# Optimization experiments

Measured on AMD Instinct MI355X. Metric: run time of the kernel, lower is better.

Reference implementation:

```python
import jax, jax.numpy as jnp
import numpy as np

K_MIN = 30.0
TAU = 1e-06
BETA = 0.9
LAMBDA_MAX = 0.1
LAMBDA_SCALE = 1.0

N, D_OUT, N_MODULES, N_CONTEXTS = 262144, 128, 64, 16


def setup_inputs() -> dict:
    key = jax.random.key(0)
    k1, k2, k3, k4 = jax.random.split(key, 4)
    Y_hat = jax.random.normal(k1, (N, D_OUT), dtype=jnp.float32)
    context_weights = jax.random.uniform(k2, (N, N_CONTEXTS), dtype=jnp.float32)
    M_pinv = jax.random.normal(k3, (N_MODULES, D_OUT), dtype=jnp.float32) * 0.1
    C_prior = jax.random.normal(k4, (N_CONTEXTS, N_MODULES, N_MODULES), dtype=jnp.float32) * 0.1
    # Buffers exactly as registered in __init__
    ema_Sigma = jnp.broadcast_to(jnp.eye(N_MODULES, dtype=jnp.float32), (N_CONTEXTS, N_MODULES, N_MODULES))
    ema_sigma_sq = jnp.ones((N_CONTEXTS, N_MODULES), dtype=jnp.float32)
    ema_initialized = jnp.zeros((N_CONTEXTS,), dtype=bool)
    return {"Y_hat": Y_hat, "context_weights": context_weights, "M_pinv": M_pinv,
            "C_prior": C_prior, "ema_Sigma": ema_Sigma, "ema_sigma_sq": ema_sigma_sq,
            "ema_initialized": ema_initialized}


def reference(Y_hat, context_weights, M_pinv, C_prior, ema_Sigma, ema_sigma_sq, ema_initialized):
    # Z_hat: [N, m]
    Z = Y_hat @ M_pinv.T
    wsum = context_weights.sum(axis=0)            # [T] == eff_n per context
    active = wsum >= K_MIN                        # context skipping, vectorized
    # Weighted mean per context: [T, m]
    mu = (context_weights.T @ Z) / wsum[:, None]
    # Weighted covariance: sum_n w_norm * (z-mu)(z-mu)^T == E_w[zz^T] - mu mu^T
    w_norm = context_weights / wsum[None, :]      # [N, T]
    S = jnp.einsum('nt,nm,nk->tmk', w_norm, Z, Z)  # [T, m, m]
    Sigma = S - mu[:, :, None] * mu[:, None, :]
    # EMA sigma_sq update (no-grad in original -> stop_gradient)
    Sigma_sg = jax.lax.stop_gradient(Sigma)
    diag_init = jnp.diagonal(Sigma_sg, axis1=1, axis2=2)                       # first-call branch
    diag_ema = jnp.diagonal(BETA * ema_Sigma + (1.0 - BETA) * Sigma_sg, axis1=1, axis2=2)
    sigma_sq = jnp.where(ema_initialized[:, None], diag_ema, diag_init)        # [T, m]
    std = jnp.sqrt(sigma_sq + TAU)
    denom = std[:, :, None] * std[:, None, :]
    C_hat = jnp.clip(Sigma / (denom + TAU), -1.0, 1.0)
    loss_t = jnp.sum((C_hat - C_prior) ** 2, axis=(1, 2)) / wsum               # [T]
    n_active = jnp.sum(active)
    total = jnp.sum(jnp.where(active, loss_t, 0.0))
    total = jnp.where(n_active > 0,
                      LAMBDA_MAX * LAMBDA_SCALE * total / jnp.maximum(n_active, 1).astype(total.dtype),
                      jnp.zeros((), total.dtype))
    return total
```

## Files before the change

### kernel.cpp

```cpp
#include <hip/hip_runtime.h>
#include <stdint.h>

#define N_ROWS 262144
#define D_OUTC 128
#define M_MOD  64
#define T_CTX  16

#define ZB_OFF   ((size_t)0)
#define ZB_BYTES ((size_t)M_MOD * N_ROWS * 2)
#define WT_OFF   (ZB_OFF + ZB_BYTES)
#define WT_BYTES ((size_t)T_CTX * N_ROWS * 2)
#define SS_OFF   (WT_OFF + WT_BYTES)
#define SS_BYTES ((size_t)T_CTX * M_MOD * M_MOD * 4)
#define B_OFF    (SS_OFF + SS_BYTES)
#define B_BYTES  ((size_t)T_CTX * M_MOD * 4)
#define WSUM_OFF (B_OFF + B_BYTES)
#define WSUM_BYTES ((size_t)64)
#define LT_OFF   (WSUM_OFF + WSUM_BYTES)
#define LT_BYTES ((size_t)64)
#define PSS_OFF  (LT_OFF + LT_BYTES)
#define PSS_BYTES ((size_t)256 * T_CTX * M_MOD * M_MOD * 2)
#define NEED_BIG (PSS_OFF + PSS_BYTES)

typedef __attribute__((ext_vector_type(4))) float f32x4;
typedef __attribute__((ext_vector_type(8))) _Float16 f16x8;
typedef __attribute__((ext_vector_type(2))) _Float16 h2;

union FR { uint4 u; f16x8 v; h2 h[4]; };

__device__ __forceinline__ float bf2f(unsigned short u) {
  return __uint_as_float(((unsigned int)u) << 16);
}
__device__ __forceinline__ unsigned short f2bf(float f) {
  unsigned int x = __float_as_uint(f);
  return (unsigned short)((x + 0x7fffu + ((x >> 16) & 1u)) >> 16);
}
__device__ __forceinline__ h2 cvt_pkrtz(float a, float b) {
  return __builtin_bit_cast(h2, __builtin_amdgcn_cvt_pkrtz(a, b));
}
#if __has_builtin(__builtin_amdgcn_fdot2)
__device__ __forceinline__ float fdot2f(h2 a, h2 b, float c) {
  return __builtin_amdgcn_fdot2(a, b, c, false);
}
#else
__device__ __forceinline__ float fdot2f(h2 a, h2 b, float c) {
  return c + (float)a[0] * (float)b[0] + (float)a[1] * (float)b[1];
}
#endif

#define WAITVM(N) asm volatile("s_waitcnt vmcnt(" #N ")" ::: "memory")
#define SBAR() do { __builtin_amdgcn_s_barrier(); __builtin_amdgcn_sched_barrier(0); } while (0)

__global__ __launch_bounds__(256, 3) void zk_kernel(
    const float* __restrict__ Y, const float* __restrict__ Mp,
    const float* __restrict__ W,
    _Float16* __restrict__ Zbt, _Float16* __restrict__ Wt)
{
  __shared__ __align__(16) float    Yl[64 * 128];
  __shared__ __align__(16) _Float16 Mpl[64 * 128];
  __shared__ float Wf[16][65];
  const int tid  = threadIdx.x;
  const int l    = tid & 63;
  const int wv   = tid >> 6;
  const int g    = l >> 4;
  const int col  = l & 15;
  const int n0   = blockIdx.x * 64;

#pragma unroll
  for (int k = 0; k < 8; ++k) {
    const int pr  = wv * 8 + k;
    const int row = pr * 2 + (l >> 5);
    const int q   = l & 31;
    const int b   = (q & ~7) | ((q & 7) ^ (row & 7));
    const float* src = Y + ((size_t)(n0 + row)) * D_OUTC + b * 4;
    __builtin_amdgcn_global_load_lds((const unsigned int*)src,
        (unsigned int*)((char*)&Yl[0] + pr * 1024), 16, 0, 0);
  }
  {
    const int m  = tid >> 2;
    const int dq = tid & 3;
#pragma unroll
    for (int i = 0; i < 4; ++i) {
      const int s = dq * 4 + i;
      const float* mp = Mp + (size_t)m * D_OUTC + s * 8;
      float4 a = *(const float4*)mp;
      float4 b = *(const float4*)(mp + 4);
      FR o;
      o.h[0] = cvt_pkrtz(a.x, a.y); o.h[1] = cvt_pkrtz(a.z, a.w);
      o.h[2] = cvt_pkrtz(b.x, b.y); o.h[3] = cvt_pkrtz(b.z, b.w);
      const int ss = (s & ~7) | ((s & 7) ^ (m & 7));
      *(uint4*)((char*)&Mpl[0] + m * 256 + ss * 16) = o.u;
    }
  }
  {
    const int r  = tid >> 2;
    const int c0 = (tid & 3) * 4;
    float4 wv4 = *(const float4*)(W + (size_t)(n0 + r) * T_CTX + c0);
    Wf[c0 + 0][r] = wv4.x; Wf[c0 + 1][r] = wv4.y;
    Wf[c0 + 2][r] = wv4.z; Wf[c0 + 3][r] = wv4.w;
  }
  __syncthreads();
  {
    const int t = tid >> 4, ni = tid & 15;
    h2 h0 = cvt_pkrtz(Wf[t][4 * ni], Wf[t][4 * ni + 1]);
    h2 h1 = cvt_pkrtz(Wf[t][4 * ni + 2], Wf[t][4 * ni + 3]);
    uint2 pk = {__builtin_bit_cast(unsigned int, h0), __builtin_bit_cast(unsigned int, h1)};
    *(uint2*)(Wt + (size_t)t * N_ROWS + n0 + 4 * ni) = pk;
  }
  f32x4 acc[4];
#pragma unroll
  for (int qi = 0; qi < 4; ++qi) acc[qi] = (f32x4){0.f, 0.f, 0.f, 0.f};
  const int nrow = wv * 16 + col;
#pragma unroll
  for (int ks = 0; ks < 4; ++ks) {
    const char* yb = (const char*)&Yl[0] + nrow * 512 + ks * 128;
    uint4 y0 = *(const uint4*)(yb + 16 * ((2 * g) ^ (nrow & 7)));
    uint4 y1 = *(const uint4*)(yb + 16 * ((2 * g + 1) ^ (nrow & 7)));
    const float* f0 = (const float*)&y0;
    const float* f1 = (const float*)&y1;
    FR B;
    B.h[0] = cvt_pkrtz(f0[0], f0[1]); B.h[1] = cvt_pkrtz(f0[2], f0[3]);
    B.h[2] = cvt_pkrtz(f1[0], f1[1]); B.h[3] = cvt_pkrtz(f1[2], f1[3]);
#pragma unroll
    for (int qi = 0; qi < 4; ++qi) {
      const int m = qi * 16 + col;
      const int s = ks * 4 + g;
      FR A;
      A.u = *(const uint4*)((char*)&Mpl[0] + m * 256 + 16 * ((s & ~7) | ((s & 7) ^ (m & 7))));
      acc[qi] = __builtin_amdgcn_mfma_f32_16x16x32_f16(A.v, B.v, acc[qi], 0, 0, 0);
    }
  }
#pragma unroll
  for (int qi = 0; qi < 4; ++qi)
#pragma unroll
    for (int i = 0; i < 4; ++i)
      Zbt[(size_t)(qi * 16 + g * 4 + i) * N_ROWS + n0 + wv * 16 + col] =
          (_Float16)acc[qi][i];
}

#define SS_NS 256
#define NCH   16
template <bool PARTIAL>
__global__ __launch_bounds__(512, 4) void ss_kernel(
    const _Float16* __restrict__ Zbt, const _Float16* __restrict__ Wt,
    float* __restrict__ SS, float* __restrict__ Bm,
    unsigned short* __restrict__ Pss)
{
  __shared__ __align__(16) _Float16 Zl[4][64 * 64];
  __shared__ __align__(16) _Float16 Wlds[8 * 1024];
  const int tid = threadIdx.x;
  const int l   = tid & 63;
  const int wv  = tid >> 6;
  const int g   = l >> 4;
  const int col = l & 15;
  const int ns  = blockIdx.x & (SS_NS - 1);
  const int cg  = blockIdx.x >> 8;
  const int ctx = cg * 8 + wv;
  const int n0b = ns * 1024;

  f32x4 acc[4][4];
  f32x4 accB[4];
#pragma unroll
  for (int a = 0; a < 4; ++a) {
    accB[a] = (f32x4){0.f, 0.f, 0.f, 0.f};
#pragma unroll
    for (int b = 0; b < 4; ++b) acc[a][b] = (f32x4){0.f, 0.f, 0.f, 0.f};
  }
  FR ones;
#pragma unroll
  for (int j = 0; j < 4; ++j) ones.h[j] = (h2){(_Float16)1.f, (_Float16)1.f};

#pragma unroll
  for (int k = 0; k < 2; ++k) {
    const _Float16* wsrc = Wt + (size_t)ctx * N_ROWS + n0b + k * 512 + l * 8;
    __builtin_amdgcn_global_load_lds((const unsigned int*)wsrc,
        (unsigned int*)((char*)&Wlds[0] + wv * 2048 + k * 1024), 16, 0, 0);
  }
  const int zrow  = 8 * wv + (l >> 3);
  const int zslot = l & 7;
  auto stage = [&](int c) {
    const int n0 = n0b + c * 64;
    const _Float16* src = Zbt + (size_t)zrow * N_ROWS + n0 + 8 * (zslot ^ (zrow & 7));
    __builtin_amdgcn_global_load_lds((const unsigned int*)src,
        (unsigned int*)((char*)&Zl[c & 3][0] + wv * 1024 + l * 16), 16, 0, 0);
  };

  stage(0); stage(1); stage(2);
  WAITVM(2);
  SBAR();

  for (int c = 0; c < NCH; ++c) {
    if (c + 3 < NCH) stage(c + 3);
    const char* zb = (const char*)&Zl[c & 3][0];
    const char* wb = (const char*)&Wlds[0] + wv * 2048 + c * 128;
#pragma unroll
    for (int s = 0; s < 2; ++s) {
      FR wfr;
      wfr.u = *(const uint4*)(wb + s * 64 + g * 16);
      FR fr[4];
#pragma unroll
      for (int qi = 0; qi < 4; ++qi) {
        const int r = qi * 16 + col;
        fr[qi].u = *(const uint4*)(zb + r * 128 + 16 * ((s * 4 + g) ^ (r & 7)));
      }
      __builtin_amdgcn_s_setprio(1);
#pragma unroll
      for (int qi = 0; qi < 4; ++qi) {
        FR A;
#pragma unroll
        for (int j = 0; j < 4; ++j) A.h[j] = fr[qi].h[j] * wfr.h[j];
        accB[qi] = __builtin_amdgcn_mfma_f32_16x16x32_f16(A.v, ones.v, accB[qi], 0, 0, 0);
#pragma unroll
        for (int ki = 0; ki < 4; ++ki)
          acc[qi][ki] = __builtin_amdgcn_mfma_f32_16x16x32_f16(A.v, fr[ki].v, acc[qi][ki], 0, 0, 0);
      }
      __builtin_amdgcn_s_setprio(0);
    }
    if (c + 3 < NCH)      { WAITVM(2); SBAR(); }
    else if (c == NCH - 3) { WAITVM(1); SBAR(); }
    else if (c == NCH - 2) { WAITVM(0); SBAR(); }
  }

  if (col == 0) {
#pragma unroll
    for (int qi = 0; qi < 4; ++qi)
#pragma unroll
      for (int i = 0; i < 4; ++i)
        atomicAdd(&Bm[ctx * 64 + qi * 16 + g * 4 + i], accB[qi][i]);
  }
  if (PARTIAL) {
    unsigned short* P = Pss + ((size_t)ns * 16 + ctx) * 4096;
#pragma unroll
    for (int qi = 0; qi < 4; ++qi)
#pragma unroll
      for (int ki = 0; ki < 4; ++ki)
#pragma unroll
        for (int i = 0; i < 4; ++i)
          P[(qi * 16 + g * 4 + i) * 64 + ki * 16 + col] = f2bf(acc[qi][ki][i]);
  } else {
#pragma unroll
    for (int qi = 0; qi < 4; ++qi)
#pragma unroll
      for (int ki = 0; ki < 4; ++ki)
#pragma unroll
        for (int i = 0; i < 4; ++i)
          atomicAdd(&SS[(size_t)ctx * 4096 + (qi * 16 + g * 4 + i) * 64 + ki * 16 + col],
                    acc[qi][ki][i]);
  }
}

__global__ __launch_bounds__(256) void wsk_kernel(const _Float16* __restrict__ Wt,
                                                  float* __restrict__ wsum)
{
  const int tid = threadIdx.x;
  const int t = blockIdx.x >> 2, q = blockIdx.x & 3;
  const uint4* base = (const uint4*)(Wt + (size_t)t * N_ROWS + q * 65536);
  const h2 one2 = {(_Float16)1.f, (_Float16)1.f};
  float s = 0.f;
  for (int i = tid; i < 8192; i += 256) {
    uint4 v = base[i];
    const h2* h = (const h2*)&v;
#pragma unroll
    for (int j = 0; j < 4; ++j) s = fdot2f(h[j], one2, s);
  }
  s += __shfl_xor(s, 1);  s += __shfl_xor(s, 2);
  s += __shfl_xor(s, 4);  s += __shfl_xor(s, 8);
  s += __shfl_xor(s, 16); s += __shfl_xor(s, 32);
  __shared__ float red[4];
  if ((tid & 63) == 0) red[tid >> 6] = s;
  __syncthreads();
  if (tid == 0) atomicAdd(&wsum[t], red[0] + red[1] + red[2] + red[3]);
}

__global__ __launch_bounds__(256) void ssred_kernel(
    const unsigned short* __restrict__ Pss, float* __restrict__ SS)
{
  const int e = blockIdx.x * 256 + threadIdx.x;
  float s = 0.f;
#pragma unroll 8
  for (int b = 0; b < 256; ++b)
    s += bf2f(Pss[(size_t)b * 65536 + e]);
  SS[e] = s;
}

__global__ __launch_bounds__(64) void fin1_kernel(
    const float* __restrict__ SS, const float* __restrict__ Bm,
    const float* __restrict__ wsum, const float* __restrict__ Cp,
    const float* __restrict__ emaS, const unsigned char* __restrict__ inited,
    float* __restrict__ LT)
{
  const int t = blockIdx.x, m = threadIdx.x;
  __shared__ float muL[64], stdL[64];
  const float ws  = wsum[t];
  const float inv = 1.0f / ws;
  const float mu  = Bm[t * 64 + m] * inv;
  {
    float Smm = SS[(size_t)t * 4096 + m * 65] * inv - mu * mu;
    float de  = 0.9f * emaS[(size_t)t * 4096 + m * 65] + 0.1f * Smm;
    float sq  = inited[t] ? de : Smm;
    muL[m]  = mu;
    stdL[m] = sqrtf(sq + 1e-6f);
  }
  __syncthreads();
  const float sm = stdL[m];
  const float* SSr = SS + (size_t)t * 4096 + m * 64;
  const float* Cpr = Cp + (size_t)t * 4096 + m * 64;
  float acc = 0.f;
#pragma unroll
  for (int k = 0; k < 64; ++k) {
    float Sig = SSr[k] * inv - mu * muL[k];
    float den = sm * stdL[k] + 1e-6f;
    float ch  = fminf(1.f, fmaxf(-1.f, Sig / den));
    float d   = ch - Cpr[k];
    acc = fmaf(d, d, acc);
  }
#pragma unroll
  for (int o = 1; o < 64; o <<= 1) acc += __shfl_xor(acc, o);
  if (m == 0) LT[t] = acc * inv;
}

__global__ __launch_bounds__(64) void fin2_kernel(
    const float* __restrict__ LT, const float* __restrict__ wsum,
    float* __restrict__ out)
{
  const int l = threadIdx.x;
  float lt = 0.f, act = 0.f;
  if (l < 16) {
    float ws = wsum[l];
    if (ws >= 30.0f) { act = 1.f; lt = LT[l]; }
  }
#pragma unroll
  for (int o = 1; o < 16; o <<= 1) {
    lt  += __shfl_xor(lt, o);
    act += __shfl_xor(act, o);
  }
  if (l == 0) out[0] = (act > 0.f) ? (0.1f * 1.0f * lt / act) : 0.f;
}

extern "C" void kernel_launch(void* const* d_in, const int* in_sizes, int n_in,
                              void* d_out, int out_size, void* d_ws, size_t ws_size,
                              hipStream_t stream) {
  (void)in_sizes; (void)n_in; (void)out_size;
  const float* Y    = (const float*)d_in[0];
  const float* W    = (const float*)d_in[1];
  const float* Mp   = (const float*)d_in[2];
  const float* Cp   = (const float*)d_in[3];
  const float* emaS = (const float*)d_in[4];
  const unsigned char* inited = (const unsigned char*)d_in[6];
  float* out = (float*)d_out;
  char* ws = (char*)d_ws;
  _Float16* Zbt = (_Float16*)(ws + ZB_OFF);
  _Float16* Wt  = (_Float16*)(ws + WT_OFF);
  float* SS   = (float*)(ws + SS_OFF);
  float* Bm   = (float*)(ws + B_OFF);
  float* wsum = (float*)(ws + WSUM_OFF);
  float* LT   = (float*)(ws + LT_OFF);
  unsigned short* Pss = (unsigned short*)(ws + PSS_OFF);

  zk_kernel<<<N_ROWS / 64, 256, 0, stream>>>(Y, Mp, W, Zbt, Wt);
  if (ws_size >= NEED_BIG) {
    (void)hipMemsetAsync(ws + B_OFF, 0, B_BYTES + WSUM_BYTES, stream);
    ss_kernel<true><<<2 * SS_NS, 512, 0, stream>>>(Zbt, Wt, SS, Bm, Pss);
    wsk_kernel<<<64, 256, 0, stream>>>(Wt, wsum);
    ssred_kernel<<<256, 256, 0, stream>>>(Pss, SS);
  } else {
    (void)hipMemsetAsync(ws + SS_OFF, 0, SS_BYTES + B_BYTES + WSUM_BYTES, stream);
    ss_kernel<false><<<2 * SS_NS, 512, 0, stream>>>(Zbt, Wt, SS, Bm, Pss);
    wsk_kernel<<<64, 256, 0, stream>>>(Wt, wsum);
  }
  fin1_kernel<<<16, 64, 0, stream>>>(SS, Bm, wsum, Cp, emaS, inited, LT);
  fin2_kernel<<<1, 64, 0, stream>>>(LT, wsum, out);
}
```

Measured before the change: 138.2 us.

## Split W transpose into its own kernel and load Y directly into registers

Moves the context-weight transpose and fp16 conversion out of the Z projection kernel into a separate wtr_kernel that writes 16-byte vector stores. The Z kernel now reads Y straight from global memory into registers instead of staging it through LDS, processes two 64-row tiles per block so the M_pinv conversion is amortised, and raises its occupancy hint to 6 blocks. This is meant to cut LDS footprint and per-block setup cost. In exchange it adds one more kernel launch, and the per-lane Y loads are less coalesced than the previous LDS-staged copy.

```diff
diff --git a/kernel.cpp b/kernel.cpp
--- a/kernel.cpp
+++ b/kernel.cpp
@@ -51,31 +51,43 @@
 #define WAITVM(N) asm volatile("s_waitcnt vmcnt(" #N ")" ::: "memory")
 #define SBAR() do { __builtin_amdgcn_s_barrier(); __builtin_amdgcn_sched_barrier(0); } while (0)
 
-__global__ __launch_bounds__(256, 3) void zk_kernel(
+__global__ __launch_bounds__(256) void wtr_kernel(const float* __restrict__ W,
+                                                  _Float16* __restrict__ Wt)
+{
+  __shared__ float Wf[16][260];
+  const int tid = threadIdx.x;
+  const int n0  = blockIdx.x * 256;
+  {
+    const float4* src = (const float4*)(W + (size_t)(n0 + tid) * T_CTX);
+#pragma unroll
+    for (int q = 0; q < 4; ++q) {
+      float4 v = src[q];
+      Wf[q * 4 + 0][tid] = v.x; Wf[q * 4 + 1][tid] = v.y;
+      Wf[q * 4 + 2][tid] = v.z; Wf[q * 4 + 3][tid] = v.w;
+    }
+  }
+  __syncthreads();
+  const int t = tid >> 4, c0 = (tid & 15) * 16;
+  FR o[2];
+#pragma unroll
+  for (int j = 0; j < 2; ++j)
+#pragma unroll
+    for (int p = 0; p < 4; ++p)
+      o[j].h[p] = cvt_pkrtz(Wf[t][c0 + j * 8 + 2 * p], Wf[t][c0 + j * 8 + 2 * p + 1]);
+  uint4* dst = (uint4*)(Wt + (size_t)t * N_ROWS + n0 + c0);
+  dst[0] = o[0].u; dst[1] = o[1].u;
+}
+
+__global__ __launch_bounds__(256, 6) void zk_kernel(
     const float* __restrict__ Y, const float* __restrict__ Mp,
-    const float* __restrict__ W,
-    _Float16* __restrict__ Zbt, _Float16* __restrict__ Wt)
-{
-  __shared__ __align__(16) float    Yl[64 * 128];
+    _Float16* __restrict__ Zbt)
+{
   __shared__ __align__(16) _Float16 Mpl[64 * 128];
-  __shared__ float Wf[16][65];
-  const int tid  = threadIdx.x;
-  const int l    = tid & 63;
-  const int wv   = tid >> 6;
-  const int g    = l >> 4;
-  const int col  = l & 15;
-  const int n0   = blockIdx.x * 64;
-
-#pragma unroll
-  for (int k = 0; k < 8; ++k) {
-    const int pr  = wv * 8 + k;
-    const int row = pr * 2 + (l >> 5);
-    const int q   = l & 31;
-    const int b   = (q & ~7) | ((q & 7) ^ (row & 7));
-    const float* src = Y + ((size_t)(n0 + row)) * D_OUTC + b * 4;
-    __builtin_amdgcn_global_load_lds((const unsigned int*)src,
-        (unsigned int*)((char*)&Yl[0] + pr * 1024), 16, 0, 0);
-  }
+  const int tid = threadIdx.x;
+  const int l   = tid & 63;
+  const int wv  = tid >> 6;
+  const int g   = l >> 4;
+  const int col = l & 15;
   {
     const int m  = tid >> 2;
     const int dq = tid & 3;
@@ -92,50 +104,44 @@
       *(uint4*)((char*)&Mpl[0] + m * 256 + ss * 16) = o.u;
     }
   }
-  {
-    const int r  = tid >> 2;
-    const int c0 = (tid & 3) * 4;
-    float4 wv4 = *(const float4*)(W + (size_t)(n0 + r) * T_CTX + c0);
-    Wf[c0 + 0][r] = wv4.x; Wf[c0 + 1][r] = wv4.y;
-    Wf[c0 + 2][r] = wv4.z; Wf[c0 + 3][r] = wv4.w;
-  }
   __syncthreads();
-  {
-    const int t = tid >> 4, ni = tid & 15;
-    h2 h0 = cvt_pkrtz(Wf[t][4 * ni], Wf[t][4 * ni + 1]);
-    h2 h1 = cvt_pkrtz(Wf[t][4 * ni + 2], Wf[t][4 * ni + 3]);
-    uint2 pk = {__builtin_bit_cast(unsigned int, h0), __builtin_bit_cast(unsigned int, h1)};
-    *(uint2*)(Wt + (size_t)t * N_ROWS + n0 + 4 * ni) = pk;
-  }
-  f32x4 acc[4];
-#pragma unroll
-  for (int qi = 0; qi < 4; ++qi) acc[qi] = (f32x4){0.f, 0.f, 0.f, 0.f};
-  const int nrow = wv * 16 + col;
-#pragma unroll
-  for (int ks = 0; ks < 4; ++ks) {
-    const char* yb = (const char*)&Yl[0] + nrow * 512 + ks * 128;
-    uint4 y0 = *(const uint4*)(yb + 16 * ((2 * g) ^ (nrow & 7)));
-    uint4 y1 = *(const uint4*)(yb + 16 * ((2 * g + 1) ^ (nrow & 7)));
-    const float* f0 = (const float*)&y0;
-    const float* f1 = (const float*)&y1;
-    FR B;
-    B.h[0] = cvt_pkrtz(f0[0], f0[1]); B.h[1] = cvt_pkrtz(f0[2], f0[3]);
-    B.h[2] = cvt_pkrtz(f1[0], f1[1]); B.h[3] = cvt_pkrtz(f1[2], f1[3]);
-#pragma unroll
-    for (int qi = 0; qi < 4; ++qi) {
-      const int m = qi * 16 + col;
-      const int s = ks * 4 + g;
-      FR A;
-      A.u = *(const uint4*)((char*)&Mpl[0] + m * 256 + 16 * ((s & ~7) | ((s & 7) ^ (m & 7))));
-      acc[qi] = __builtin_amdgcn_mfma_f32_16x16x32_f16(A.v, B.v, acc[qi], 0, 0, 0);
-    }
-  }
-#pragma unroll
-  for (int qi = 0; qi < 4; ++qi)
-#pragma unroll
-    for (int i = 0; i < 4; ++i)
-      Zbt[(size_t)(qi * 16 + g * 4 + i) * N_ROWS + n0 + wv * 16 + col] =
-          (_Float16)acc[qi][i];
+#pragma unroll
+  for (int it = 0; it < 2; ++it) {
+    const int n0 = (blockIdx.x * 2 + it) * 64;
+    const int nr = n0 + wv * 16 + col;
+    const float* __restrict__ yr = Y + (size_t)nr * D_OUTC;
+    float4 yv[8];
+#pragma unroll
+    for (int ks = 0; ks < 4; ++ks) {
+      yv[2 * ks]     = *(const float4*)(yr + ks * 32 + g * 8);
+      yv[2 * ks + 1] = *(const float4*)(yr + ks * 32 + g * 8 + 4);
+    }
+    f32x4 acc[4];
+#pragma unroll
+    for (int qi = 0; qi < 4; ++qi) acc[qi] = (f32x4){0.f, 0.f, 0.f, 0.f};
+#pragma unroll
+    for (int ks = 0; ks < 4; ++ks) {
+      const float* f0 = (const float*)&yv[2 * ks];
+      const float* f1 = (const float*)&yv[2 * ks + 1];
+      FR B;
+      B.h[0] = cvt_pkrtz(f0[0], f0[1]); B.h[1] = cvt_pkrtz(f0[2], f0[3]);
+      B.h[2] = cvt_pkrtz(f1[0], f1[1]); B.h[3] = cvt_pkrtz(f1[2], f1[3]);
+#pragma unroll
+      for (int qi = 0; qi < 4; ++qi) {
+        const int m = qi * 16 + col;
+        const int s = ks * 4 + g;
+        FR A;
+        A.u = *(const uint4*)((char*)&Mpl[0] + m * 256 + 16 * ((s & ~7) | ((s & 7) ^ (m & 7))));
+        acc[qi] = __builtin_amdgcn_mfma_f32_16x16x32_f16(A.v, B.v, acc[qi], 0, 0, 0);
+      }
+    }
+#pragma unroll
+    for (int qi = 0; qi < 4; ++qi)
+#pragma unroll
+      for (int i = 0; i < 4; ++i)
+        Zbt[(size_t)(qi * 16 + g * 4 + i) * N_ROWS + n0 + wv * 16 + col] =
+            (_Float16)acc[qi][i];
+  }
 }
 
 #define SS_NS 256
@@ -216,7 +222,7 @@
       }
       __builtin_amdgcn_s_setprio(0);
     }
-    if (c + 3 < NCH)      { WAITVM(2); SBAR(); }
+    if (c + 3 < NCH)       { WAITVM(2); SBAR(); }
     else if (c == NCH - 3) { WAITVM(1); SBAR(); }
     else if (c == NCH - 2) { WAITVM(0); SBAR(); }
   }
@@ -357,7 +363,8 @@
   float* LT   = (float*)(ws + LT_OFF);
   unsigned short* Pss = (unsigned short*)(ws + PSS_OFF);
 
-  zk_kernel<<<N_ROWS / 64, 256, 0, stream>>>(Y, Mp, W, Zbt, Wt);
+  wtr_kernel<<<N_ROWS / 256, 256, 0, stream>>>(W, Wt);
+  zk_kernel<<<N_ROWS / 128, 256, 0, stream>>>(Y, Mp, Zbt);
   if (ws_size >= NEED_BIG) {
     (void)hipMemsetAsync(ws + B_OFF, 0, B_BYTES + WSUM_BYTES, stream);
     ss_kernel<true><<<2 * SS_NS, 512, 0, stream>>>(Zbt, Wt, SS, Bm, Pss);
```

Result: no change. 139.7 us (+1.1%).
